# Optimization experiments

Hardware: AMD Instinct MI355X
Metric: run time of the kernel (lower is better)

## Reference

```python
import jax, jax.numpy as jnp
import numpy as np

N_NODES = 50000
ELU_ALPHA = 0.2  # torch.nn.ELU(0.2): alpha=0.2


def _elu(v, alpha):
    return jnp.where(v > 0, v, alpha * jnp.expm1(v))


def setup_inputs() -> dict:
    key = jax.random.key(0)
    k1, k2, k3, k4, k5 = jax.random.split(key, 5)
    fin, H, F = 128, 4, 32
    E = 1600000
    return {
        "x": jax.random.normal(k1, (N_NODES, fin), dtype=jnp.float32),
        "W": jax.random.normal(k2, (fin, H * F), dtype=jnp.float32) * (1.414 / np.sqrt(fin)),
        "a_src": jax.random.normal(k3, (H, F), dtype=jnp.float32) * 0.1,
        "a_tgt": jax.random.normal(k4, (H, F), dtype=jnp.float32) * 0.1,
        "edge_index": jax.random.randint(k5, (E, 2), 0, N_NODES, dtype=jnp.int64),
    }


def reference(x, W, a_src, a_tgt, edge_index):
    # GAT layer (dropout omitted: eval mode). x: [N, fin]
    N = x.shape[0]
    H, F = a_src.shape
    xp = (x @ W).reshape(N, H, F)                 # projected node feats [N,H,F]
    s_src = jnp.einsum("nhf,hf->nh", xp, a_src)   # per-head source scores [N,H]
    s_tgt = jnp.einsum("nhf,hf->nh", xp, a_tgt)   # per-head target scores [N,H]

    src = edge_index[:, 0]
    tgt = edge_index[:, 1]

    # edge-wise gather (the memory-bound hotspot)
    e = _elu(s_src[src] + s_tgt[tgt], ELU_ALPHA)  # [E,H]

    # segment softmax over edges sharing a target node
    m = jax.ops.segment_max(e, tgt, num_segments=N)           # [N,H]
    m = jnp.where(jnp.isfinite(m), m, 0.0)
    ex = jnp.exp(e - m[tgt])                                  # [E,H]
    denom = jax.ops.segment_sum(ex, tgt, num_segments=N)      # [N,H]
    alpha = ex / denom[tgt]                                   # [E,H]

    # gather source features, weight, scatter-add into target nodes
    msg = alpha[:, :, None] * xp[src]                          # [E,H,F]
    out = jax.ops.segment_sum(msg, tgt, num_segments=N)        # [N,H,F]
    return out.reshape(N, H * F)                               # concat heads
```

## Files before the change

### kernel.cpp

```cpp
#include <hip/hip_runtime.h>
#include <hip/hip_bf16.h>
#include <math.h>

#define FIN 128
#define NHEAD 4
#define CH 128
#define ELU_A 0.2f

#define BSHIFT 8
#define NB 196
#define CAP 16384
#define T_EDGES 2048

typedef unsigned int uint32;
typedef __attribute__((ext_vector_type(8))) short short8;
typedef __attribute__((ext_vector_type(4))) float f32x4;

__device__ __forceinline__ float bf16lo(uint32 u) {
    union { uint32 i; float f; } c; c.i = u << 16; return c.f;
}
__device__ __forceinline__ float bf16hi(uint32 u) {
    union { uint32 i; float f; } c; c.i = u & 0xffff0000u; return c.f;
}
__device__ __forceinline__ unsigned short f2b(float f) {
    union { float f; uint32 u; } c; c.f = f;
    uint32 u = c.u;
    return (unsigned short)((u + 0x7fffu + ((u >> 16) & 1u)) >> 16);
}

__global__ __launch_bounds__(256) void partition_kernel(
    const int2* __restrict__ ei2, int* __restrict__ bcnt,
    uint32* __restrict__ ebuck, const float* __restrict__ W,
    unsigned short* __restrict__ Wt, int E)
{
    if (blockIdx.x == gridDim.x - 1) {
        for (int task = threadIdx.x; task < CH * (FIN / 8); task += 256) {
            int n  = task >> 4;
            int k0 = (task & 15) * 8;
            unsigned short v[8];
#pragma unroll
            for (int j = 0; j < 8; ++j) v[j] = f2b(W[(size_t)(k0 + j) * CH + n]);
            *(uint4*)&Wt[(size_t)n * FIN + k0] = *(uint4*)v;
        }
        return;
    }

    __shared__ uint32 stage[T_EDGES];
    __shared__ int hist[256], scanbuf[256], loff[256], cnt2[256], base[256];
    const int tid = threadIdx.x;
    const int e0 = blockIdx.x * T_EDGES;
    const int tile = min(T_EDGES, E - e0);

    hist[tid] = 0; cnt2[tid] = 0;
    __syncthreads();

    uint32 rec[8];
#pragma unroll
    for (int j = 0; j < 8; ++j) {
        int idx = e0 + j * 256 + tid;
        if (idx < E) {
            int2 p = ei2[idx];
            rec[j] = (uint32)p.x | ((uint32)p.y << 16);
            atomicAdd(&hist[p.y >> BSHIFT], 1);
        } else rec[j] = 0xFFFFFFFFu;
    }
    __syncthreads();

    scanbuf[tid] = hist[tid];
    __syncthreads();
    for (int off = 1; off < 256; off <<= 1) {
        int v = (tid >= off) ? scanbuf[tid - off] : 0;
        __syncthreads();
        scanbuf[tid] += v;
        __syncthreads();
    }
    loff[tid] = scanbuf[tid] - hist[tid];
    if (tid < NB && hist[tid] > 0)
        base[tid] = tid * CAP + atomicAdd(&bcnt[tid], hist[tid]);
    __syncthreads();

#pragma unroll
    for (int j = 0; j < 8; ++j) {
        if (rec[j] != 0xFFFFFFFFu) {
            int b = rec[j] >> (16 + BSHIFT);
            int r = atomicAdd(&cnt2[b], 1);
            stage[loff[b] + r] = rec[j];
        }
    }
    __syncthreads();

    for (int i = tid; i < tile; i += 256) {
        uint32 rc = stage[i];
        int b = rc >> (16 + BSHIFT);
        ebuck[(size_t)base[b] + (i - loff[b])] = rc;
    }
}

__global__ __launch_bounds__(256) void gemm_bscan_kernel(
    const float* __restrict__ x, const unsigned short* __restrict__ Wt,
    unsigned short* __restrict__ xpb, const float* __restrict__ a_src,
    const float* __restrict__ a_tgt, float* __restrict__ s_src,
    float* __restrict__ s_tgt, const int* __restrict__ bcnt,
    int* __restrict__ bbase, int N)
{
    __shared__ unsigned short cbuf[4][16][132];

    if (blockIdx.x == gridDim.x - 1) {
        int* s = (int*)&cbuf[0][0][0];
        const int t = threadIdx.x;
        int v = (t < NB) ? bcnt[t] : 0;
        s[t] = v;
        __syncthreads();
        for (int off = 1; off < 256; off <<= 1) {
            int u = (t >= off) ? s[t - off] : 0;
            __syncthreads();
            s[t] += u;
            __syncthreads();
        }
        if (t < NB) bbase[t] = s[t] - v;
        return;
    }

    const int lane = threadIdx.x & 63;
    const int wid  = threadIdx.x >> 6;
    const int rowbase = blockIdx.x * 64 + wid * 16;

    const int rr   = min(rowbase + (lane & 15), N - 1);
    const int krow = (lane >> 4) * 8;

    f32x4 acc[8];
#pragma unroll
    for (int c = 0; c < 8; ++c) acc[c] = (f32x4){0.f, 0.f, 0.f, 0.f};

#pragma unroll
    for (int s = 0; s < 4; ++s) {
        const int koff = s * 32 + krow;
        const float* xr = x + (size_t)rr * FIN + koff;
        float4 p0 = *(const float4*)xr;
        float4 p1 = *(const float4*)(xr + 4);
        short8 af;
        af[0] = (short)f2b(p0.x); af[1] = (short)f2b(p0.y);
        af[2] = (short)f2b(p0.z); af[3] = (short)f2b(p0.w);
        af[4] = (short)f2b(p1.x); af[5] = (short)f2b(p1.y);
        af[6] = (short)f2b(p1.z); af[7] = (short)f2b(p1.w);
#pragma unroll
        for (int c = 0; c < 8; ++c) {
            const short8 bf = *(const short8*)&Wt[(size_t)(c * 16 + (lane & 15)) * FIN + koff];
            acc[c] = __builtin_amdgcn_mfma_f32_16x16x32_bf16(af, bf, acc[c], 0, 0, 0);
        }
    }

#pragma unroll
    for (int c = 0; c < 8; ++c)
#pragma unroll
        for (int r = 0; r < 4; ++r)
            cbuf[wid][(lane >> 4) * 4 + r][c * 16 + (lane & 15)] = f2b(acc[c][r]);
    __syncthreads();

    for (int r = 0; r < 16; ++r) {
        int row = rowbase + r;
        if (row < N) {
            uint32 v = *(const uint32*)&cbuf[wid][r][lane * 2];
            *(uint32*)&xpb[(size_t)row * CH + lane * 2] = v;
        }
    }

    {
        const int srow = lane >> 2;
        const int sh   = lane & 3;
        const unsigned short* cp = &cbuf[wid][srow][sh * 32];
        const float* as = a_src + sh * 32;
        const float* at = a_tgt + sh * 32;
        float ps = 0.f, pt = 0.f;
#pragma unroll
        for (int q = 0; q < 4; ++q) {
            uint4 u = *(const uint4*)&cp[q * 8];
            float4 a0 = *(const float4*)&as[q * 8];
            float4 a1 = *(const float4*)&as[q * 8 + 4];
            float4 b0 = *(const float4*)&at[q * 8];
            float4 b1 = *(const float4*)&at[q * 8 + 4];
            float l0 = bf16lo(u.x), h0 = bf16hi(u.x);
            float l1 = bf16lo(u.y), h1 = bf16hi(u.y);
            float l2 = bf16lo(u.z), h2 = bf16hi(u.z);
            float l3 = bf16lo(u.w), h3 = bf16hi(u.w);
            ps += l0*a0.x + h0*a0.y + l1*a0.z + h1*a0.w
                + l2*a1.x + h2*a1.y + l3*a1.z + h3*a1.w;
            pt += l0*b0.x + h0*b0.y + l1*b0.z + h1*b0.w
                + l2*b1.x + h2*b1.y + l3*b1.z + h3*b1.w;
        }
        int node = rowbase + srow;
        if (node < N) {
            s_src[(size_t)node * NHEAD + sh] = ps;
            s_tgt[(size_t)node * NHEAD + sh] = pt;
        }
    }
}

__global__ __launch_bounds__(1024) void fine_scatter_kernel(
    const uint32* __restrict__ ebuck, const int* __restrict__ bcnt,
    const int* __restrict__ bbase, int* __restrict__ deg,
    int* __restrict__ rowptr, int* __restrict__ srcs, int N)
{
    __shared__ int ldeg[256], psum[256], lcur[256];
    const int b = blockIdx.x;
    const int tid = threadIdx.x;
    if (tid < 256) ldeg[tid] = 0;
    __syncthreads();

    const int cnt = bcnt[b];
    const uint32* rp = ebuck + (size_t)b * CAP;

    for (int i = tid; i < cnt; i += 1024)
        atomicAdd(&ldeg[(rp[i] >> 16) & 255], 1);
    __syncthreads();

    if (tid < 256) psum[tid] = ldeg[tid];
    __syncthreads();
    for (int off = 1; off < 256; off <<= 1) {
        int u = 0;
        if (tid < 256 && tid >= off) u = psum[tid - off];
        __syncthreads();
        if (tid < 256) psum[tid] += u;
        __syncthreads();
    }

    const int gb = bbase[b];
    if (tid < 256) {
        int pref = gb + psum[tid] - ldeg[tid];
        lcur[tid] = pref;
        int node = b * 256 + tid;
        if (node < N) { deg[node] = ldeg[tid]; rowptr[node] = pref; }
    }
    __syncthreads();

    for (int i = tid; i < cnt; i += 1024) {
        uint32 rc = rp[i];
        int pos = atomicAdd(&lcur[(rc >> 16) & 255], 1);
        srcs[pos] = rc & 0xffff;
    }
}

__global__ __launch_bounds__(256) void aggregate_kernel(
    const int* __restrict__ srcs, const int* __restrict__ rowptr,
    const int* __restrict__ deg, const float* __restrict__ s_src,
    const float* __restrict__ s_tgt, const uint32* __restrict__ xpb,
    float* __restrict__ out, int N)
{
    const int lane = threadIdx.x & 63;
    const int wid  = __builtin_amdgcn_readfirstlane(threadIdx.x >> 6);
    const int t = blockIdx.x * 4 + wid;
    if (t >= N) return;

    const int start = __builtin_amdgcn_readfirstlane(rowptr[t]);
    const int d     = __builtin_amdgcn_readfirstlane(deg[t]);
    const int h     = lane >> 4;
    const int cj    = lane & 7;
    const int chh   = (lane >> 3) & 3;

    const float st_c = s_tgt[(size_t)t * NHEAD + chh];
    const float st_h = s_tgt[(size_t)t * NHEAD + h];
    const int bb = h * 8;

    float accx = 0.0f, accy = 0.0f, dsum = 0.0f;
    int k = 0;

    for (; k + 8 <= d; k += 8) {
        int   sv = srcs[start + k + cj];
        float a  = s_src[(size_t)sv * NHEAD + chh];
        float v  = a + st_c;
        float u  = v > 0.0f ? v : ELU_A * (__expf(v) - 1.0f);
        float e  = __expf(u);

        int s0 = srcs[start + k + 0], s1 = srcs[start + k + 1];
        int s2 = srcs[start + k + 2], s3 = srcs[start + k + 3];
        int s4 = srcs[start + k + 4], s5 = srcs[start + k + 5];
        int s6 = srcs[start + k + 6], s7 = srcs[start + k + 7];

        uint32 x0 = xpb[(size_t)s0 * 64 + lane];
        uint32 x1 = xpb[(size_t)s1 * 64 + lane];
        uint32 x2 = xpb[(size_t)s2 * 64 + lane];
        uint32 x3 = xpb[(size_t)s3 * 64 + lane];
        uint32 x4 = xpb[(size_t)s4 * 64 + lane];
        uint32 x5 = xpb[(size_t)s5 * 64 + lane];
        uint32 x6 = xpb[(size_t)s6 * 64 + lane];
        uint32 x7 = xpb[(size_t)s7 * 64 + lane];

        float e0 = __shfl(e, bb + 0), e1 = __shfl(e, bb + 1);
        float e2 = __shfl(e, bb + 2), e3 = __shfl(e, bb + 3);
        float e4 = __shfl(e, bb + 4), e5 = __shfl(e, bb + 5);
        float e6 = __shfl(e, bb + 6), e7 = __shfl(e, bb + 7);

#define ACC(E, X) { dsum += (E); accx += (E) * bf16lo(X); accy += (E) * bf16hi(X); }
        ACC(e0, x0) ACC(e1, x1) ACC(e2, x2) ACC(e3, x3)
        ACC(e4, x4) ACC(e5, x5) ACC(e6, x6) ACC(e7, x7)
#undef ACC
    }

    for (; k < d; ++k) {
        int   s  = srcs[start + k];
        float a  = s_src[(size_t)s * NHEAD + h];
        uint32 xv = xpb[(size_t)s * 64 + lane];
        float v = a + st_h;
        float u = v > 0.0f ? v : ELU_A * (__expf(v) - 1.0f);
        float e = __expf(u);
        dsum += e; accx += e * bf16lo(xv); accy += e * bf16hi(xv);
    }

    float inv = (d > 0) ? 1.0f / dsum : 0.0f;
    float2 o = make_float2(accx * inv, accy * inv);
    *(float2*)&out[(size_t)t * CH + lane * 2] = o;
}

extern "C" void kernel_launch(void* const* d_in, const int* in_sizes, int n_in,
                              void* d_out, int out_size, void* d_ws, size_t ws_size,
                              hipStream_t stream)
{
    const float* x     = (const float*)d_in[0];
    const float* W     = (const float*)d_in[1];
    const float* a_src = (const float*)d_in[2];
    const float* a_tgt = (const float*)d_in[3];
    const int*   ei    = (const int*)d_in[4];

    const int N = in_sizes[0] / FIN;
    const int E = in_sizes[4] / 2;
    const int PB = (E + T_EDGES - 1) / T_EDGES;
    const int GB = (N + 63) / 64;

    char* ws = (char*)d_ws;
    unsigned short* xpb = (unsigned short*)ws;  ws += (size_t)N * CH * sizeof(unsigned short);
    unsigned short* Wt  = (unsigned short*)ws;  ws += (size_t)FIN * CH * sizeof(unsigned short);
    float* s_src  = (float*)ws;                 ws += (size_t)N * NHEAD * sizeof(float);
    float* s_tgt  = (float*)ws;                 ws += (size_t)N * NHEAD * sizeof(float);
    int*   deg    = (int*)ws;                   ws += (size_t)N * sizeof(int);
    int*   bcnt   = (int*)ws;                   ws += (size_t)NB * sizeof(int);
    int*   bbase  = (int*)ws;                   ws += (size_t)NB * sizeof(int);
    int*   rowptr = (int*)ws;                   ws += (size_t)N * sizeof(int);
    int*   srcs   = (int*)ws;                   ws += (size_t)E * sizeof(int);
    uint32* ebuck = (uint32*)ws;                ws += (size_t)NB * CAP * sizeof(uint32);

    float* out = (float*)d_out;
    const int2* ei2 = (const int2*)ei;

    hipMemsetAsync(bcnt, 0, (size_t)NB * sizeof(int), stream);

    partition_kernel<<<PB + 1, 256, 0, stream>>>(ei2, bcnt, ebuck, W, Wt, E);
    gemm_bscan_kernel<<<GB + 1, 256, 0, stream>>>(
        x, Wt, xpb, a_src, a_tgt, s_src, s_tgt, bcnt, bbase, N);
    fine_scatter_kernel<<<NB, 1024, 0, stream>>>(
        ebuck, bcnt, bbase, deg, rowptr, srcs, N);
    aggregate_kernel<<<(N + 3) / 4, 256, 0, stream>>>(
        srcs, rowptr, deg, s_src, s_tgt, (const uint32*)xpb, out, N);
}
```

Before: 134.4 us.

## Fuse partition and GEMM into one launch, move bucket scan, widen aggregate unroll

Merges the edge-partition kernel and the projection GEMM into a single grid. Each GEMM block now converts W to bf16 and transposes it in shared memory itself, which removes the separate Wt buffer and lets the two independent phases overlap in one launch. The bucket-base prefix scan is dropped; each fine_scatter block instead sums the preceding bucket counts with a small reduction. The aggregate kernel gains a 16-edge unrolled loop ahead of the 8-edge loop to raise memory-level parallelism. In exchange, every GEMM block redoes the W conversion, and the wider loop uses more registers.

```diff
diff --git a/kernel.cpp b/kernel.cpp
--- a/kernel.cpp
+++ b/kernel.cpp
@@ -28,102 +28,91 @@
     return (unsigned short)((u + 0x7fffu + ((u >> 16) & 1u)) >> 16);
 }
 
-__global__ __launch_bounds__(256) void partition_kernel(
+union SMem {
+    struct {
+        uint32 stage[T_EDGES];
+        int hist[256], scanbuf[256], loff[256], cnt2[256], base[256];
+    } p;
+    unsigned short wt[128][136];
+    unsigned short cbuf[4][16][132];
+};
+
+__global__ __launch_bounds__(256) void mega_kernel(
     const int2* __restrict__ ei2, int* __restrict__ bcnt,
-    uint32* __restrict__ ebuck, const float* __restrict__ W,
-    unsigned short* __restrict__ Wt, int E)
+    uint32* __restrict__ ebuck, const float* __restrict__ x,
+    const float* __restrict__ W, unsigned short* __restrict__ xpb,
+    const float* __restrict__ a_src, const float* __restrict__ a_tgt,
+    float* __restrict__ s_src, float* __restrict__ s_tgt,
+    int E, int N, int PB)
 {
-    if (blockIdx.x == gridDim.x - 1) {
-        for (int task = threadIdx.x; task < CH * (FIN / 8); task += 256) {
-            int n  = task >> 4;
-            int k0 = (task & 15) * 8;
-            unsigned short v[8];
-#pragma unroll
-            for (int j = 0; j < 8; ++j) v[j] = f2b(W[(size_t)(k0 + j) * CH + n]);
-            *(uint4*)&Wt[(size_t)n * FIN + k0] = *(uint4*)v;
+    __shared__ SMem sm;
+    const int tid = threadIdx.x;
+
+    if ((int)blockIdx.x < PB) {
+        const int e0 = blockIdx.x * T_EDGES;
+        const int tile = min(T_EDGES, E - e0);
+
+        sm.p.hist[tid] = 0; sm.p.cnt2[tid] = 0;
+        __syncthreads();
+
+        uint32 rec[8];
+#pragma unroll
+        for (int j = 0; j < 8; ++j) {
+            int idx = e0 + j * 256 + tid;
+            if (idx < E) {
+                int2 p = ei2[idx];
+                rec[j] = (uint32)p.x | ((uint32)p.y << 16);
+                atomicAdd(&sm.p.hist[p.y >> BSHIFT], 1);
+            } else rec[j] = 0xFFFFFFFFu;
+        }
+        __syncthreads();
+
+        sm.p.scanbuf[tid] = sm.p.hist[tid];
+        __syncthreads();
+        for (int off = 1; off < 256; off <<= 1) {
+            int v = (tid >= off) ? sm.p.scanbuf[tid - off] : 0;
+            __syncthreads();
+            sm.p.scanbuf[tid] += v;
+            __syncthreads();
+        }
+        sm.p.loff[tid] = sm.p.scanbuf[tid] - sm.p.hist[tid];
+        if (tid < NB && sm.p.hist[tid] > 0)
+            sm.p.base[tid] = tid * CAP + atomicAdd(&bcnt[tid], sm.p.hist[tid]);
+        __syncthreads();
+
+#pragma unroll
+        for (int j = 0; j < 8; ++j) {
+            if (rec[j] != 0xFFFFFFFFu) {
+                int b = rec[j] >> (16 + BSHIFT);
+                int r = atomicAdd(&sm.p.cnt2[b], 1);
+                sm.p.stage[sm.p.loff[b] + r] = rec[j];
+            }
+        }
+        __syncthreads();
+
+        for (int i = tid; i < tile; i += 256) {
+            uint32 rc = sm.p.stage[i];
+            int b = rc >> (16 + BSHIFT);
+            ebuck[(size_t)sm.p.base[b] + (i - sm.p.loff[b])] = rc;
         }
         return;
     }
 
-    __shared__ uint32 stage[T_EDGES];
-    __shared__ int hist[256], scanbuf[256], loff[256], cnt2[256], base[256];
-    const int tid = threadIdx.x;
-    const int e0 = blockIdx.x * T_EDGES;
-    const int tile = min(T_EDGES, E - e0);
-
-    hist[tid] = 0; cnt2[tid] = 0;
-    __syncthreads();
-
-    uint32 rec[8];
-#pragma unroll
-    for (int j = 0; j < 8; ++j) {
-        int idx = e0 + j * 256 + tid;
-        if (idx < E) {
-            int2 p = ei2[idx];
-            rec[j] = (uint32)p.x | ((uint32)p.y << 16);
-            atomicAdd(&hist[p.y >> BSHIFT], 1);
-        } else rec[j] = 0xFFFFFFFFu;
-    }
-    __syncthreads();
-
-    scanbuf[tid] = hist[tid];
-    __syncthreads();
-    for (int off = 1; off < 256; off <<= 1) {
-        int v = (tid >= off) ? scanbuf[tid - off] : 0;
-        __syncthreads();
-        scanbuf[tid] += v;
-        __syncthreads();
-    }
-    loff[tid] = scanbuf[tid] - hist[tid];
-    if (tid < NB && hist[tid] > 0)
-        base[tid] = tid * CAP + atomicAdd(&bcnt[tid], hist[tid]);
-    __syncthreads();
-
-#pragma unroll
-    for (int j = 0; j < 8; ++j) {
-        if (rec[j] != 0xFFFFFFFFu) {
-            int b = rec[j] >> (16 + BSHIFT);
-            int r = atomicAdd(&cnt2[b], 1);
-            stage[loff[b] + r] = rec[j];
-        }
-    }
-    __syncthreads();
-
-    for (int i = tid; i < tile; i += 256) {
-        uint32 rc = stage[i];
-        int b = rc >> (16 + BSHIFT);
-        ebuck[(size_t)base[b] + (i - loff[b])] = rc;
-    }
-}
-
-__global__ __launch_bounds__(256) void gemm_bscan_kernel(
-    const float* __restrict__ x, const unsigned short* __restrict__ Wt,
-    unsigned short* __restrict__ xpb, const float* __restrict__ a_src,
-    const float* __restrict__ a_tgt, float* __restrict__ s_src,
-    float* __restrict__ s_tgt, const int* __restrict__ bcnt,
-    int* __restrict__ bbase, int N)
-{
-    __shared__ unsigned short cbuf[4][16][132];
-
-    if (blockIdx.x == gridDim.x - 1) {
-        int* s = (int*)&cbuf[0][0][0];
-        const int t = threadIdx.x;
-        int v = (t < NB) ? bcnt[t] : 0;
-        s[t] = v;
-        __syncthreads();
-        for (int off = 1; off < 256; off <<= 1) {
-            int u = (t >= off) ? s[t - off] : 0;
-            __syncthreads();
-            s[t] += u;
-            __syncthreads();
-        }
-        if (t < NB) bbase[t] = s[t] - v;
-        return;
-    }
-
-    const int lane = threadIdx.x & 63;
-    const int wid  = threadIdx.x >> 6;
-    const int rowbase = blockIdx.x * 64 + wid * 16;
+    const int gb = blockIdx.x - PB;
+
+    for (int i = tid; i < FIN * CH / 2; i += 256) {
+        int n  = i & 127;
+        int k2 = i >> 7;
+        float w0 = W[(size_t)(2 * k2 + 0) * CH + n];
+        float w1 = W[(size_t)(2 * k2 + 1) * CH + n];
+        uint32 pk = (uint32)f2b(w0) | ((uint32)f2b(w1) << 16);
+        *(uint32*)&sm.wt[n][2 * k2] = pk;
+    }
+    __syncthreads();
+
+    const int lane = tid & 63;
+    const int wid  = tid >> 6;
+    const int rowbase = gb * 64 + wid * 16;
 
     const int rr   = min(rowbase + (lane & 15), N - 1);
     const int krow = (lane >> 4) * 8;
@@ -145,22 +134,23 @@
         af[6] = (short)f2b(p1.z); af[7] = (short)f2b(p1.w);
 #pragma unroll
         for (int c = 0; c < 8; ++c) {
-            const short8 bf = *(const short8*)&Wt[(size_t)(c * 16 + (lane & 15)) * FIN + koff];
+            const short8 bf = *(const short8*)&sm.wt[c * 16 + (lane & 15)][koff];
             acc[c] = __builtin_amdgcn_mfma_f32_16x16x32_bf16(af, bf, acc[c], 0, 0, 0);
         }
     }
+    __syncthreads();
 
 #pragma unroll
     for (int c = 0; c < 8; ++c)
 #pragma unroll
         for (int r = 0; r < 4; ++r)
-            cbuf[wid][(lane >> 4) * 4 + r][c * 16 + (lane & 15)] = f2b(acc[c][r]);
+            sm.cbuf[wid][(lane >> 4) * 4 + r][c * 16 + (lane & 15)] = f2b(acc[c][r]);
     __syncthreads();
 
     for (int r = 0; r < 16; ++r) {
         int row = rowbase + r;
         if (row < N) {
-            uint32 v = *(const uint32*)&cbuf[wid][r][lane * 2];
+            uint32 v = *(const uint32*)&sm.cbuf[wid][r][lane * 2];
             *(uint32*)&xpb[(size_t)row * CH + lane * 2] = v;
         }
     }
@@ -168,7 +158,7 @@
     {
         const int srow = lane >> 2;
         const int sh   = lane & 3;
-        const unsigned short* cp = &cbuf[wid][srow][sh * 32];
+        const unsigned short* cp = &sm.cbuf[wid][srow][sh * 32];
         const float* as = a_src + sh * 32;
         const float* at = a_tgt + sh * 32;
         float ps = 0.f, pt = 0.f;
@@ -198,14 +188,23 @@
 
 __global__ __launch_bounds__(1024) void fine_scatter_kernel(
     const uint32* __restrict__ ebuck, const int* __restrict__ bcnt,
-    const int* __restrict__ bbase, int* __restrict__ deg,
-    int* __restrict__ rowptr, int* __restrict__ srcs, int N)
+    int* __restrict__ deg, int* __restrict__ rowptr,
+    int* __restrict__ srcs, int N)
 {
-    __shared__ int ldeg[256], psum[256], lcur[256];
+    __shared__ int ldeg[256], psum[256], lcur[256], red[256];
     const int b = blockIdx.x;
     const int tid = threadIdx.x;
-    if (tid < 256) ldeg[tid] = 0;
-    __syncthreads();
+
+    if (tid < 256) {
+        red[tid]  = (tid < b) ? bcnt[tid] : 0;
+        ldeg[tid] = 0;
+    }
+    __syncthreads();
+    for (int off = 128; off >= 1; off >>= 1) {
+        if (tid < off) red[tid] += red[tid + off];
+        __syncthreads();
+    }
+    const int gb = red[0];
 
     const int cnt = bcnt[b];
     const uint32* rp = ebuck + (size_t)b * CAP;
@@ -224,7 +223,6 @@
         __syncthreads();
     }
 
-    const int gb = bbase[b];
     if (tid < 256) {
         int pref = gb + psum[tid] - ldeg[tid];
         lcur[tid] = pref;
@@ -254,18 +252,61 @@
     const int start = __builtin_amdgcn_readfirstlane(rowptr[t]);
     const int d     = __builtin_amdgcn_readfirstlane(deg[t]);
     const int h     = lane >> 4;
-    const int cj    = lane & 7;
-    const int chh   = (lane >> 3) & 3;
-
-    const float st_c = s_tgt[(size_t)t * NHEAD + chh];
     const float st_h = s_tgt[(size_t)t * NHEAD + h];
-    const int bb = h * 8;
 
     float accx = 0.0f, accy = 0.0f, dsum = 0.0f;
     int k = 0;
 
+#define ACC(E, X) { dsum += (E); accx += (E) * bf16lo(X); accy += (E) * bf16hi(X); }
+
+    const int cj16 = lane & 15;
+    const int bb16 = h * 16;
+    for (; k + 16 <= d; k += 16) {
+        int   sv = srcs[start + k + cj16];
+        float a  = s_src[(size_t)sv * NHEAD + h];
+        float v  = a + st_h;
+        float u  = v > 0.0f ? v : ELU_A * (__expf(v) - 1.0f);
+        float e  = __expf(u);
+
+        int s0 = srcs[start + k + 0],  s1 = srcs[start + k + 1];
+        int s2 = srcs[start + k + 2],  s3 = srcs[start + k + 3];
+        int s4 = srcs[start + k + 4],  s5 = srcs[start + k + 5];
+        int s6 = srcs[start + k + 6],  s7 = srcs[start + k + 7];
+        int s8 = srcs[start + k + 8],  s9 = srcs[start + k + 9];
+        int sa = srcs[start + k + 10], sb = srcs[start + k + 11];
+        int sc = srcs[start + k + 12], sd = srcs[start + k + 13];
+        int se = srcs[start + k + 14], sf = srcs[start + k + 15];
+
+        uint32 x0 = xpb[(size_t)s0 * 64 + lane], x1 = xpb[(size_t)s1 * 64 + lane];
+        uint32 x2 = xpb[(size_t)s2 * 64 + lane], x3 = xpb[(size_t)s3 * 64 + lane];
+        uint32 x4 = xpb[(size_t)s4 * 64 + lane], x5 = xpb[(size_t)s5 * 64 + lane];
+        uint32 x6 = xpb[(size_t)s6 * 64 + lane], x7 = xpb[(size_t)s7 * 64 + lane];
+        uint32 x8 = xpb[(size_t)s8 * 64 + lane], x9 = xpb[(size_t)s9 * 64 + lane];
+        uint32 xa = xpb[(size_t)sa * 64 + lane], xb = xpb[(size_t)sb * 64 + lane];
+        uint32 xc = xpb[(size_t)sc * 64 + lane], xd = xpb[(size_t)sd * 64 + lane];
+        uint32 xe = xpb[(size_t)se * 64 + lane], xf = xpb[(size_t)sf * 64 + lane];
+
+        float e0 = __shfl(e, bb16 + 0),  e1 = __shfl(e, bb16 + 1);
+        float e2 = __shfl(e, bb16 + 2),  e3 = __shfl(e, bb16 + 3);
+        float e4 = __shfl(e, bb16 + 4),  e5 = __shfl(e, bb16 + 5);
+        float e6 = __shfl(e, bb16 + 6),  e7 = __shfl(e, bb16 + 7);
+        float e8 = __shfl(e, bb16 + 8),  e9 = __shfl(e, bb16 + 9);
+        float ea = __shfl(e, bb16 + 10), eb = __shfl(e, bb16 + 11);
+        float ec = __shfl(e, bb16 + 12), ed = __shfl(e, bb16 + 13);
+        float ee = __shfl(e, bb16 + 14), ef = __shfl(e, bb16 + 15);
+
+        ACC(e0, x0) ACC(e1, x1) ACC(e2, x2) ACC(e3, x3)
+        ACC(e4, x4) ACC(e5, x5) ACC(e6, x6) ACC(e7, x7)
+        ACC(e8, x8) ACC(e9, x9) ACC(ea, xa) ACC(eb, xb)
+        ACC(ec, xc) ACC(ed, xd) ACC(ee, xe) ACC(ef, xf)
+    }
+
+    const int cj8 = lane & 7;
+    const int chh = (lane >> 3) & 3;
+    const float st_c = s_tgt[(size_t)t * NHEAD + chh];
+    const int bb8 = h * 8;
     for (; k + 8 <= d; k += 8) {
-        int   sv = srcs[start + k + cj];
+        int   sv = srcs[start + k + cj8];
         float a  = s_src[(size_t)sv * NHEAD + chh];
         float v  = a + st_c;
         float u  = v > 0.0f ? v : ELU_A * (__expf(v) - 1.0f);
@@ -276,24 +317,18 @@
         int s4 = srcs[start + k + 4], s5 = srcs[start + k + 5];
         int s6 = srcs[start + k + 6], s7 = srcs[start + k + 7];
 
-        uint32 x0 = xpb[(size_t)s0 * 64 + lane];
-        uint32 x1 = xpb[(size_t)s1 * 64 + lane];
-        uint32 x2 = xpb[(size_t)s2 * 64 + lane];
-        uint32 x3 = xpb[(size_t)s3 * 64 + lane];
-        uint32 x4 = xpb[(size_t)s4 * 64 + lane];
-        uint32 x5 = xpb[(size_t)s5 * 64 + lane];
-        uint32 x6 = xpb[(size_t)s6 * 64 + lane];
-        uint32 x7 = xpb[(size_t)s7 * 64 + lane];
-
-        float e0 = __shfl(e, bb + 0), e1 = __shfl(e, bb + 1);
-        float e2 = __shfl(e, bb + 2), e3 = __shfl(e, bb + 3);
-        float e4 = __shfl(e, bb + 4), e5 = __shfl(e, bb + 5);
-        float e6 = __shfl(e, bb + 6), e7 = __shfl(e, bb + 7);
-
-#define ACC(E, X) { dsum += (E); accx += (E) * bf16lo(X); accy += (E) * bf16hi(X); }
+        uint32 x0 = xpb[(size_t)s0 * 64 + lane], x1 = xpb[(size_t)s1 * 64 + lane];
+        uint32 x2 = xpb[(size_t)s2 * 64 + lane], x3 = xpb[(size_t)s3 * 64 + lane];
+        uint32 x4 = xpb[(size_t)s4 * 64 + lane], x5 = xpb[(size_t)s5 * 64 + lane];
+        uint32 x6 = xpb[(size_t)s6 * 64 + lane], x7 = xpb[(size_t)s7 * 64 + lane];
+
+        float e0 = __shfl(e, bb8 + 0), e1 = __shfl(e, bb8 + 1);
+        float e2 = __shfl(e, bb8 + 2), e3 = __shfl(e, bb8 + 3);
+        float e4 = __shfl(e, bb8 + 4), e5 = __shfl(e, bb8 + 5);
+        float e6 = __shfl(e, bb8 + 6), e7 = __shfl(e, bb8 + 7);
+
         ACC(e0, x0) ACC(e1, x1) ACC(e2, x2) ACC(e3, x3)
         ACC(e4, x4) ACC(e5, x5) ACC(e6, x6) ACC(e7, x7)
-#undef ACC
     }
 
     for (; k < d; ++k) {
@@ -303,8 +338,9 @@
         float v = a + st_h;
         float u = v > 0.0f ? v : ELU_A * (__expf(v) - 1.0f);
         float e = __expf(u);
-        dsum += e; accx += e * bf16lo(xv); accy += e * bf16hi(xv);
-    }
+        ACC(e, xv)
+    }
+#undef ACC
 
     float inv = (d > 0) ? 1.0f / dsum : 0.0f;
     float2 o = make_float2(accx * inv, accy * inv);
@@ -328,12 +364,10 @@
 
     char* ws = (char*)d_ws;
     unsigned short* xpb = (unsigned short*)ws;  ws += (size_t)N * CH * sizeof(unsigned short);
-    unsigned short* Wt  = (unsigned short*)ws;  ws += (size_t)FIN * CH * sizeof(unsigned short);
     float* s_src  = (float*)ws;                 ws += (size_t)N * NHEAD * sizeof(float);
     float* s_tgt  = (float*)ws;                 ws += (size_t)N * NHEAD * sizeof(float);
     int*   deg    = (int*)ws;                   ws += (size_t)N * sizeof(int);
     int*   bcnt   = (int*)ws;                   ws += (size_t)NB * sizeof(int);
-    int*   bbase  = (int*)ws;                   ws += (size_t)NB * sizeof(int);
     int*   rowptr = (int*)ws;                   ws += (size_t)N * sizeof(int);
     int*   srcs   = (int*)ws;                   ws += (size_t)E * sizeof(int);
     uint32* ebuck = (uint32*)ws;                ws += (size_t)NB * CAP * sizeof(uint32);
@@ -343,11 +377,10 @@
 
     hipMemsetAsync(bcnt, 0, (size_t)NB * sizeof(int), stream);
 
-    partition_kernel<<<PB + 1, 256, 0, stream>>>(ei2, bcnt, ebuck, W, Wt, E);
-    gemm_bscan_kernel<<<GB + 1, 256, 0, stream>>>(
-        x, Wt, xpb, a_src, a_tgt, s_src, s_tgt, bcnt, bbase, N);
+    mega_kernel<<<PB + GB, 256, 0, stream>>>(
+        ei2, bcnt, ebuck, x, W, xpb, a_src, a_tgt, s_src, s_tgt, E, N, PB);
     fine_scatter_kernel<<<NB, 1024, 0, stream>>>(
-        ebuck, bcnt, bbase, deg, rowptr, srcs, N);
+        ebuck, bcnt, deg, rowptr, srcs, N);
     aggregate_kernel<<<(N + 3) / 4, 256, 0, stream>>>(
         srcs, rowptr, deg, s_src, s_tgt, (const uint32*)xpb, out, N);
 }
```

Result: faster. 120.5 us (-10.4%).
